# Kernel tuning notes

Measured on AMD Instinct MI355X. Metric: run time of the kernel, lower is better.

Reference implementation:

```python
import jax, jax.numpy as jnp
import numpy as np

B, S, D, H = 4, 2048, 1024, 16
DK = D // H


def setup_inputs() -> dict:
    key = jax.random.key(0)
    ks = jax.random.split(key, 7)
    s = 1.0 / np.sqrt(D)
    return {
        "q": jax.random.normal(ks[0], (B, S, D), jnp.float32),
        "k": jax.random.normal(ks[1], (B, S, D), jnp.float32),
        "v": jax.random.normal(ks[2], (B, S, D), jnp.float32),
        "Wq": jax.random.normal(ks[3], (D, D), jnp.float32) * s,
        "Wk": jax.random.normal(ks[4], (D, D), jnp.float32) * s,
        "Wv": jax.random.normal(ks[5], (D, D), jnp.float32) * s,
        "Wo": jax.random.normal(ks[6], (D, D), jnp.float32) * s,
    }


def _split(x):
    # [B,S,D] -> [B,H,S,DK]
    return x.reshape(B, S, H, DK).transpose(0, 2, 1, 3)


def reference(q, k, v, Wq, Wk, Wv, Wo):
    # Linear projections (nn.Linear with bias=False: x @ W^T)
    qh = _split(q @ Wq.T)
    kh = _split(k @ Wk.T)
    vh = _split(v @ Wv.T)
    scale = 1.0 / jnp.sqrt(jnp.asarray(DK, qh.dtype))
    # attention scores [B,H,S,S]
    attn = jnp.einsum("bhqd,bhkd->bhqk", qh, kh) * scale
    # causal mask: disallow k > q
    causal = jnp.tril(jnp.ones((S, S), dtype=bool))
    attn = jnp.where(causal[None, None], attn, -jnp.inf)
    attn = jax.nn.softmax(attn, axis=-1)  # dropout p=0.0 -> identity
    out = jnp.einsum("bhqk,bhkd->bhqd", attn, vh)
    # combine heads [B,H,S,DK] -> [B,S,D]
    out = out.transpose(0, 2, 1, 3).reshape(B, S, D)
    return out @ Wo.T
```

## Files before the change

kernel.cpp:

```cpp
#include <hip/hip_runtime.h>
#include <math.h>
#include <stdint.h>

#define B_  4
#define S_  2048
#define D_  1024
#define H_  16
#define DK_ 64
#define NR_ (B_ * S_)

typedef _Float16 half8  __attribute__((ext_vector_type(8)));
typedef _Float16 half4  __attribute__((ext_vector_type(4)));
typedef float    floatx4 __attribute__((ext_vector_type(4)));

#define GBN 128
#define GBM 64
#define GBK 32
#define LDH 40

__global__ __launch_bounds__(256)
void gemm_xwt_mfma(const float* __restrict__ X, const float* __restrict__ W,
                   void* __restrict__ outp, int mode) {
    __shared__ __align__(16) _Float16 Xhi[GBN][LDH];
    __shared__ __align__(16) _Float16 Xlo[GBN][LDH];
    __shared__ __align__(16) _Float16 Whi[GBM][LDH];
    __shared__ __align__(16) _Float16 Wlo[GBM][LDH];
    const int K = D_;

    const int tid  = threadIdx.x;
    const int wave = tid >> 6;
    const int lane = tid & 63;
    const int row16 = lane & 15;
    const int quad  = lane >> 4;
    const int n0 = blockIdx.x * GBN;
    const int m0 = blockIdx.y * GBM;

    floatx4 acc[2][4];
    const floatx4 zero4 = {0.f, 0.f, 0.f, 0.f};
    #pragma unroll
    for (int i = 0; i < 2; ++i)
        #pragma unroll
        for (int j = 0; j < 4; ++j) acc[i][j] = zero4;

    for (int k0 = 0; k0 < K; k0 += GBK) {
        __syncthreads();
        #pragma unroll
        for (int i = 0; i < 4; ++i) {
            const int t   = i * 256 + tid;
            const int row = t >> 3;
            const int c4  = (t & 7) << 2;
            float4 xv = *(const float4*)(X + (size_t)(n0 + row) * K + k0 + c4);
            float f[4] = {xv.x, xv.y, xv.z, xv.w};
            #pragma unroll
            for (int c = 0; c < 4; ++c) {
                _Float16 h = (_Float16)f[c];
                Xhi[row][c4 + c] = h;
                Xlo[row][c4 + c] = (_Float16)(f[c] - (float)h);
            }
        }
        #pragma unroll
        for (int i = 0; i < 2; ++i) {
            const int t   = i * 256 + tid;
            const int row = t >> 3;
            const int c4  = (t & 7) << 2;
            float4 wv = *(const float4*)(W + (size_t)(m0 + row) * K + k0 + c4);
            float f[4] = {wv.x, wv.y, wv.z, wv.w};
            #pragma unroll
            for (int c = 0; c < 4; ++c) {
                _Float16 h = (_Float16)f[c];
                Whi[row][c4 + c] = h;
                Wlo[row][c4 + c] = (_Float16)(f[c] - (float)h);
            }
        }
        __syncthreads();

        half8 a_hi[2], a_lo[2], b_hi[4], b_lo[4];
        #pragma unroll
        for (int ni = 0; ni < 2; ++ni) {
            const int r = wave * 32 + ni * 16 + row16;
            a_hi[ni] = *(const half8*)&Xhi[r][quad * 8];
            a_lo[ni] = *(const half8*)&Xlo[r][quad * 8];
        }
        #pragma unroll
        for (int mj = 0; mj < 4; ++mj) {
            const int r = mj * 16 + row16;
            b_hi[mj] = *(const half8*)&Whi[r][quad * 8];
            b_lo[mj] = *(const half8*)&Wlo[r][quad * 8];
        }

        #pragma unroll
        for (int ni = 0; ni < 2; ++ni)
            #pragma unroll
            for (int mj = 0; mj < 4; ++mj) {
                acc[ni][mj] = __builtin_amdgcn_mfma_f32_16x16x32_f16(
                    a_hi[ni], b_hi[mj], acc[ni][mj], 0, 0, 0);
                acc[ni][mj] = __builtin_amdgcn_mfma_f32_16x16x32_f16(
                    a_hi[ni], b_lo[mj], acc[ni][mj], 0, 0, 0);
                acc[ni][mj] = __builtin_amdgcn_mfma_f32_16x16x32_f16(
                    a_lo[ni], b_hi[mj], acc[ni][mj], 0, 0, 0);
            }
    }

    #pragma unroll
    for (int ni = 0; ni < 2; ++ni)
        #pragma unroll
        for (int mj = 0; mj < 4; ++mj) {
            if (mode == 2) {
                const int s  = n0 + wave * 32 + ni * 16 + quad * 4;
                const int b  = s >> 11;
                const int sr = s & (S_ - 1);
                const int m  = m0 + mj * 16 + row16;
                const int h  = m >> 6;
                const int dk = m & 63;
                float4 v4 = make_float4(acc[ni][mj][0], acc[ni][mj][1],
                                        acc[ni][mj][2], acc[ni][mj][3]);
                *(float4*)((float*)outp +
                           (((size_t)b * H_ + h) * DK_ + dk) * S_ + sr) = v4;
            } else {
                #pragma unroll
                for (int rg = 0; rg < 4; ++rg) {
                    const int n = n0 + wave * 32 + ni * 16 + quad * 4 + rg;
                    const int m = m0 + mj * 16 + row16;
                    const float v = acc[ni][mj][rg];
                    if (mode == 0) {
                        ((float*)outp)[(size_t)n * D_ + m] = v;
                    } else {
                        const int b  = n >> 11;
                        const int s  = n & (S_ - 1);
                        const int h  = m >> 6;
                        const int dk = m & 63;
                        union { _Float16 h16; uint16_t u; } hi, lo;
                        hi.h16 = (_Float16)v;
                        lo.h16 = (_Float16)(v - (float)hi.h16);
                        uint32_t u = ((uint32_t)lo.u << 16) | (uint32_t)hi.u;
                        ((uint32_t*)outp)[(((size_t)b * H_ + h) * S_ + s) * DK_ + dk] = u;
                    }
                }
            }
        }
}

__global__ __launch_bounds__(256)
void attn_mfma(const uint32_t* __restrict__ Qhl, const uint32_t* __restrict__ Khl,
               const float* __restrict__ Vt, float* __restrict__ A) {
    __shared__ __align__(16) _Float16 KhiC[64][64];
    __shared__ __align__(16) _Float16 KloC[64][64];
    __shared__ __align__(16) _Float16 VC[64][64];
    __shared__ __align__(16) _Float16 PCT[4][16][72];

    const int bh = blockIdx.y;
    const int qt = (int)(gridDim.x - 1) - (int)blockIdx.x;
    const int q0 = qt * 64;
    const int tid  = threadIdx.x;
    const int wave = tid >> 6;
    const int lane = tid & 63;
    const int c    = lane & 15;
    const int quad = lane >> 4;

    const uint32_t* Kb = Khl + (size_t)bh * S_ * DK_;
    const float*    Vb = Vt  + (size_t)bh * DK_ * S_;

    half8 qhi[2], qlo[2];
    {
        const uint32_t* Qrow = Qhl + ((size_t)bh * S_ + q0 + wave * 16 + c) * DK_;
        #pragma unroll
        for (int ks = 0; ks < 2; ++ks) {
            uint32_t u[8];
            *(uint4*)&u[0] = *(const uint4*)(Qrow + ks * 32 + quad * 8);
            *(uint4*)&u[4] = *(const uint4*)(Qrow + ks * 32 + quad * 8 + 4);
            union { half8 v; uint16_t s[8]; } hi, lo;
            #pragma unroll
            for (int j = 0; j < 8; ++j) {
                hi.s[j] = (uint16_t)(u[j] & 0xffffu);
                lo.s[j] = (uint16_t)(u[j] >> 16);
            }
            qhi[ks] = hi.v; qlo[ks] = lo.v;
        }
    }

    floatx4 acc_o[4];
    const floatx4 zero4 = {0.f, 0.f, 0.f, 0.f};
    #pragma unroll
    for (int dt = 0; dt < 4; ++dt) acc_o[dt] = zero4;
    float mrun = -INFINITY, lrun = 0.f;

    const int srow = tid >> 2;
    const int soff = (tid & 3) * 16;
    const int ch0  = (tid & 3) * 2;

    uint4 ku[4];
    float4 vf[4];
    auto load_tile = [&](int kt) {
        const uint4* ksrc = (const uint4*)(Kb + (size_t)(kt * 64 + srow) * DK_ + soff);
        ku[0] = ksrc[0]; ku[1] = ksrc[1]; ku[2] = ksrc[2]; ku[3] = ksrc[3];
        const float4* vsrc = (const float4*)(Vb + (size_t)srow * S_ + kt * 64 + soff);
        vf[0] = vsrc[0]; vf[1] = vsrc[1]; vf[2] = vsrc[2]; vf[3] = vsrc[3];
    };
    auto write_tile = [&]() {
        #pragma unroll
        for (int hf = 0; hf < 2; ++hf) {
            const int swz = ((ch0 + hf) ^ (srow & 7)) * 8;
            uint32_t uu[8];
            *(uint4*)&uu[0] = ku[2 * hf];
            *(uint4*)&uu[4] = ku[2 * hf + 1];
            union { half8 v; uint16_t s[8]; } hi, lo;
            #pragma unroll
            for (int j = 0; j < 8; ++j) {
                hi.s[j] = (uint16_t)(uu[j] & 0xffffu);
                lo.s[j] = (uint16_t)(uu[j] >> 16);
            }
            *(half8*)&KhiC[srow][swz] = hi.v;
            *(half8*)&KloC[srow][swz] = lo.v;
            union { half8 v; _Float16 h[8]; } vt;
            float4 a = vf[2 * hf], b = vf[2 * hf + 1];
            vt.h[0] = (_Float16)a.x; vt.h[1] = (_Float16)a.y;
            vt.h[2] = (_Float16)a.z; vt.h[3] = (_Float16)a.w;
            vt.h[4] = (_Float16)b.x; vt.h[5] = (_Float16)b.y;
            vt.h[6] = (_Float16)b.z; vt.h[7] = (_Float16)b.w;
            *(half8*)&VC[srow][swz] = vt.v;
        }
    };

    const int qmy = q0 + wave * 16 + c;
    const floatx4 neg4 = {-INFINITY, -INFINITY, -INFINITY, -INFINITY};

    load_tile(0);
    write_tile();

    for (int kt = 0; kt <= qt; ++kt) {
        const int k0 = kt * 64;
        const bool diag = (kt == qt);
        __syncthreads();
        if (kt < qt) load_tile(kt + 1);

        floatx4 sc[4];
        #pragma unroll
        for (int t = 0; t < 4; ++t) {
            if (diag && t > wave) { sc[t] = neg4; continue; }
            floatx4 s4 = zero4;
            const int krow = t * 16 + c;
            #pragma unroll
            for (int ks = 0; ks < 2; ++ks) {
                const int swz = ((ks * 4 + quad) ^ (krow & 7)) * 8;
                half8 kb = *(const half8*)&KhiC[krow][swz];
                half8 kl = *(const half8*)&KloC[krow][swz];
                s4 = __builtin_amdgcn_mfma_f32_16x16x32_f16(kb, qhi[ks], s4, 0, 0, 0);
                s4 = __builtin_amdgcn_mfma_f32_16x16x32_f16(kl, qhi[ks], s4, 0, 0, 0);
                s4 = __builtin_amdgcn_mfma_f32_16x16x32_f16(kb, qlo[ks], s4, 0, 0, 0);
            }
            #pragma unroll
            for (int r = 0; r < 4; ++r) s4[r] *= 0.125f;
            if (diag && t == wave) {
                #pragma unroll
                for (int r = 0; r < 4; ++r) {
                    const int k = k0 + t * 16 + quad * 4 + r;
                    if (k > qmy) s4[r] = -INFINITY;
                }
            }
            sc[t] = s4;
        }

        float mx = -INFINITY;
        #pragma unroll
        for (int t = 0; t < 4; ++t)
            #pragma unroll
            for (int r = 0; r < 4; ++r) mx = fmaxf(mx, sc[t][r]);
        mx = fmaxf(mx, __shfl_xor(mx, 16));
        mx = fmaxf(mx, __shfl_xor(mx, 32));
        const float mnew  = fmaxf(mrun, mx);
        const float alpha = __expf(mrun - mnew);
        float ls = 0.f;
        #pragma unroll
        for (int t = 0; t < 4; ++t) {
            half4 p4;
            #pragma unroll
            for (int r = 0; r < 4; ++r) {
                const float p = __expf(sc[t][r] - mnew);
                ls += p;
                p4[r] = (_Float16)p;
            }
            *(half4*)&PCT[wave][c][t * 16 + quad * 4] = p4;
        }
        lrun = alpha * lrun + ls;
        mrun = mnew;
        #pragma unroll
        for (int dt = 0; dt < 4; ++dt)
            #pragma unroll
            for (int r = 0; r < 4; ++r) acc_o[dt][r] *= alpha;

        #pragma unroll
        for (int kc = 0; kc < 2; ++kc) {
            if (diag && kc == 1 && wave < 2) continue;
            half8 pb = *(const half8*)&PCT[wave][c][kc * 32 + quad * 8];
            #pragma unroll
            for (int dt = 0; dt < 4; ++dt) {
                const int vrow = dt * 16 + c;
                const int swz = ((kc * 4 + quad) ^ (vrow & 7)) * 8;
                half8 va = *(const half8*)&VC[vrow][swz];
                acc_o[dt] = __builtin_amdgcn_mfma_f32_16x16x32_f16(va, pb, acc_o[dt], 0, 0, 0);
            }
        }

        __syncthreads();
        if (kt < qt) write_tile();
    }

    float l = lrun;
    l += __shfl_xor(l, 16);
    l += __shfl_xor(l, 32);
    const float inv = 1.f / l;
    const int b = bh >> 4, h = bh & 15;
    float* dst = A + ((size_t)b * S_ + qmy) * D_ + h * DK_;
    #pragma unroll
    for (int dt = 0; dt < 4; ++dt) {
        float4 o4 = make_float4(acc_o[dt][0] * inv, acc_o[dt][1] * inv,
                                acc_o[dt][2] * inv, acc_o[dt][3] * inv);
        *(float4*)(dst + dt * 16 + quad * 4) = o4;
    }
}

extern "C" void kernel_launch(void* const* d_in, const int* in_sizes, int n_in,
                              void* d_out, int out_size, void* d_ws, size_t ws_size,
                              hipStream_t stream) {
    const float* q  = (const float*)d_in[0];
    const float* k  = (const float*)d_in[1];
    const float* v  = (const float*)d_in[2];
    const float* Wq = (const float*)d_in[3];
    const float* Wk = (const float*)d_in[4];
    const float* Wv = (const float*)d_in[5];
    const float* Wo = (const float*)d_in[6];
    float* out = (float*)d_out;

    const size_t SZ = (size_t)B_ * S_ * D_;
    float* wsf = (float*)d_ws;
    uint32_t* Qhl = (uint32_t*)wsf;
    uint32_t* Khl = (uint32_t*)(wsf + SZ);
    float*    Vt  = wsf + 2 * SZ;
    float*    A   = wsf + 3 * SZ;

    dim3 gb(NR_ / GBN, D_ / GBM);
    gemm_xwt_mfma<<<gb, 256, 0, stream>>>(q, Wq, Qhl, 1);
    gemm_xwt_mfma<<<gb, 256, 0, stream>>>(k, Wk, Khl, 1);
    gemm_xwt_mfma<<<gb, 256, 0, stream>>>(v, Wv, Vt, 2);

    dim3 ga(S_ / 64, B_ * H_);
    attn_mfma<<<ga, 256, 0, stream>>>(Qhl, Khl, Vt, A);

    gemm_xwt_mfma<<<gb, 256, 0, stream>>>(A, Wo, out, 0);
}
```

Baseline: 697.7 us.

## Pre-split inputs to fp16 hi/lo in separate kernels and prefetch GEMM tiles

Adds a split kernel that converts fp32 activations and weights into separate fp16 hi and lo arrays, so the GEMM no longer converts inside its main loop and can load fp16 tiles directly, with register prefetch of the next K tile. Intermediates (Q/K hi-lo, V transposed, attention output hi-lo) are stored as planar fp16, which halves V storage and removes unpacking in the attention kernel. The cost is seven extra split launches and extra global round-trips for the split activations, plus V rounded to fp16 at the GEMM output.

```diff
diff --git a/kernel.cpp b/kernel.cpp
--- a/kernel.cpp
+++ b/kernel.cpp
@@ -13,14 +13,35 @@
 typedef _Float16 half4  __attribute__((ext_vector_type(4)));
 typedef float    floatx4 __attribute__((ext_vector_type(4)));
 
+__global__ __launch_bounds__(256)
+void split_f32(const float* __restrict__ src, _Float16* __restrict__ hi,
+               _Float16* __restrict__ lo, int n8) {
+    const int i = blockIdx.x * 256 + threadIdx.x;
+    if (i >= n8) return;
+    const float4* s4 = (const float4*)src;
+    float4 a = s4[2 * i];
+    float4 b = s4[2 * i + 1];
+    float f[8] = {a.x, a.y, a.z, a.w, b.x, b.y, b.z, b.w};
+    union { half8 v; _Float16 h[8]; } H, L;
+    #pragma unroll
+    for (int j = 0; j < 8; ++j) {
+        _Float16 h = (_Float16)f[j];
+        H.h[j] = h;
+        L.h[j] = (_Float16)(f[j] - (float)h);
+    }
+    *(half8*)(hi + (size_t)i * 8) = H.v;
+    *(half8*)(lo + (size_t)i * 8) = L.v;
+}
+
 #define GBN 128
 #define GBM 64
 #define GBK 32
 #define LDH 40
 
 __global__ __launch_bounds__(256)
-void gemm_xwt_mfma(const float* __restrict__ X, const float* __restrict__ W,
-                   void* __restrict__ outp, int mode) {
+void gemm_xwt_mfma(const _Float16* __restrict__ Xh, const _Float16* __restrict__ Xl,
+                   const _Float16* __restrict__ Wh, const _Float16* __restrict__ Wl,
+                   void* __restrict__ out0, void* __restrict__ out1, int mode) {
     __shared__ __align__(16) _Float16 Xhi[GBN][LDH];
     __shared__ __align__(16) _Float16 Xlo[GBN][LDH];
     __shared__ __align__(16) _Float16 Whi[GBM][LDH];
@@ -35,6 +56,11 @@
     const int n0 = blockIdx.x * GBN;
     const int m0 = blockIdx.y * GBM;
 
+    const int xrow = tid >> 1;
+    const int xc   = (tid & 1) << 4;
+    const int wrow = tid >> 2;
+    const int wc   = (tid & 3) << 3;
+
     floatx4 acc[2][4];
     const floatx4 zero4 = {0.f, 0.f, 0.f, 0.f};
     #pragma unroll
@@ -42,37 +68,31 @@
         #pragma unroll
         for (int j = 0; j < 4; ++j) acc[i][j] = zero4;
 
+    uint4 xh0, xh1, xl0, xl1, wh0, wl0;
+    auto load_regs = [&](int k0) {
+        const _Float16* ph = Xh + (size_t)(n0 + xrow) * K + k0 + xc;
+        const _Float16* pl = Xl + (size_t)(n0 + xrow) * K + k0 + xc;
+        xh0 = *(const uint4*)ph;
+        xh1 = *(const uint4*)(ph + 8);
+        xl0 = *(const uint4*)pl;
+        xl1 = *(const uint4*)(pl + 8);
+        const _Float16* pwh = Wh + (size_t)(m0 + wrow) * K + k0 + wc;
+        const _Float16* pwl = Wl + (size_t)(m0 + wrow) * K + k0 + wc;
+        wh0 = *(const uint4*)pwh;
+        wl0 = *(const uint4*)pwl;
+    };
+
+    load_regs(0);
     for (int k0 = 0; k0 < K; k0 += GBK) {
         __syncthreads();
-        #pragma unroll
-        for (int i = 0; i < 4; ++i) {
-            const int t   = i * 256 + tid;
-            const int row = t >> 3;
-            const int c4  = (t & 7) << 2;
-            float4 xv = *(const float4*)(X + (size_t)(n0 + row) * K + k0 + c4);
-            float f[4] = {xv.x, xv.y, xv.z, xv.w};
-            #pragma unroll
-            for (int c = 0; c < 4; ++c) {
-                _Float16 h = (_Float16)f[c];
-                Xhi[row][c4 + c] = h;
-                Xlo[row][c4 + c] = (_Float16)(f[c] - (float)h);
-            }
-        }
-        #pragma unroll
-        for (int i = 0; i < 2; ++i) {
-            const int t   = i * 256 + tid;
-            const int row = t >> 3;
-            const int c4  = (t & 7) << 2;
-            float4 wv = *(const float4*)(W + (size_t)(m0 + row) * K + k0 + c4);
-            float f[4] = {wv.x, wv.y, wv.z, wv.w};
-            #pragma unroll
-            for (int c = 0; c < 4; ++c) {
-                _Float16 h = (_Float16)f[c];
-                Whi[row][c4 + c] = h;
-                Wlo[row][c4 + c] = (_Float16)(f[c] - (float)h);
-            }
-        }
+        *(uint4*)&Xhi[xrow][xc]     = xh0;
+        *(uint4*)&Xhi[xrow][xc + 8] = xh1;
+        *(uint4*)&Xlo[xrow][xc]     = xl0;
+        *(uint4*)&Xlo[xrow][xc + 8] = xl1;
+        *(uint4*)&Whi[wrow][wc]     = wh0;
+        *(uint4*)&Wlo[wrow][wc]     = wl0;
         __syncthreads();
+        if (k0 + GBK < K) load_regs(k0 + GBK);
 
         half8 a_hi[2], a_lo[2], b_hi[4], b_lo[4];
         #pragma unroll
@@ -112,10 +132,11 @@
                 const int m  = m0 + mj * 16 + row16;
                 const int h  = m >> 6;
                 const int dk = m & 63;
-                float4 v4 = make_float4(acc[ni][mj][0], acc[ni][mj][1],
-                                        acc[ni][mj][2], acc[ni][mj][3]);
-                *(float4*)((float*)outp +
-                           (((size_t)b * H_ + h) * DK_ + dk) * S_ + sr) = v4;
+                half4 h4;
+                #pragma unroll
+                for (int r = 0; r < 4; ++r) h4[r] = (_Float16)acc[ni][mj][r];
+                *(half4*)((_Float16*)out0 +
+                          (((size_t)b * H_ + h) * DK_ + dk) * S_ + sr) = h4;
             } else {
                 #pragma unroll
                 for (int rg = 0; rg < 4; ++rg) {
@@ -123,17 +144,17 @@
                     const int m = m0 + mj * 16 + row16;
                     const float v = acc[ni][mj][rg];
                     if (mode == 0) {
-                        ((float*)outp)[(size_t)n * D_ + m] = v;
+                        ((float*)out0)[(size_t)n * D_ + m] = v;
                     } else {
                         const int b  = n >> 11;
                         const int s  = n & (S_ - 1);
                         const int h  = m >> 6;
                         const int dk = m & 63;
-                        union { _Float16 h16; uint16_t u; } hi, lo;
-                        hi.h16 = (_Float16)v;
-                        lo.h16 = (_Float16)(v - (float)hi.h16);
-                        uint32_t u = ((uint32_t)lo.u << 16) | (uint32_t)hi.u;
-                        ((uint32_t*)outp)[(((size_t)b * H_ + h) * S_ + s) * DK_ + dk] = u;
+                        _Float16 hi16 = (_Float16)v;
+                        _Float16 lo16 = (_Float16)(v - (float)hi16);
+                        const size_t idx = (((size_t)b * H_ + h) * S_ + s) * DK_ + dk;
+                        ((_Float16*)out0)[idx] = hi16;
+                        ((_Float16*)out1)[idx] = lo16;
                     }
                 }
             }
@@ -141,8 +162,10 @@
 }
 
 __global__ __launch_bounds__(256)
-void attn_mfma(const uint32_t* __restrict__ Qhl, const uint32_t* __restrict__ Khl,
-               const float* __restrict__ Vt, float* __restrict__ A) {
+void attn_mfma(const _Float16* __restrict__ Qhi_g, const _Float16* __restrict__ Qlo_g,
+               const _Float16* __restrict__ Khi_g, const _Float16* __restrict__ Klo_g,
+               const _Float16* __restrict__ Vth,
+               _Float16* __restrict__ Ahi, _Float16* __restrict__ Alo) {
     __shared__ __align__(16) _Float16 KhiC[64][64];
     __shared__ __align__(16) _Float16 KloC[64][64];
     __shared__ __align__(16) _Float16 VC[64][64];
@@ -157,24 +180,18 @@
     const int c    = lane & 15;
     const int quad = lane >> 4;
 
-    const uint32_t* Kb = Khl + (size_t)bh * S_ * DK_;
-    const float*    Vb = Vt  + (size_t)bh * DK_ * S_;
+    const _Float16* Kbh = Khi_g + (size_t)bh * S_ * DK_;
+    const _Float16* Kbl = Klo_g + (size_t)bh * S_ * DK_;
+    const _Float16* Vb  = Vth   + (size_t)bh * DK_ * S_;
 
     half8 qhi[2], qlo[2];
     {
-        const uint32_t* Qrow = Qhl + ((size_t)bh * S_ + q0 + wave * 16 + c) * DK_;
+        const _Float16* Qrh = Qhi_g + ((size_t)bh * S_ + q0 + wave * 16 + c) * DK_;
+        const _Float16* Qrl = Qlo_g + ((size_t)bh * S_ + q0 + wave * 16 + c) * DK_;
         #pragma unroll
         for (int ks = 0; ks < 2; ++ks) {
-            uint32_t u[8];
-            *(uint4*)&u[0] = *(const uint4*)(Qrow + ks * 32 + quad * 8);
-            *(uint4*)&u[4] = *(const uint4*)(Qrow + ks * 32 + quad * 8 + 4);
-            union { half8 v; uint16_t s[8]; } hi, lo;
-            #pragma unroll
-            for (int j = 0; j < 8; ++j) {
-                hi.s[j] = (uint16_t)(u[j] & 0xffffu);
-                lo.s[j] = (uint16_t)(u[j] >> 16);
-            }
-            qhi[ks] = hi.v; qlo[ks] = lo.v;
+            qhi[ks] = *(const half8*)(Qrh + ks * 32 + quad * 8);
+            qlo[ks] = *(const half8*)(Qrl + ks * 32 + quad * 8);
         }
     }
 
@@ -188,36 +205,22 @@
     const int soff = (tid & 3) * 16;
     const int ch0  = (tid & 3) * 2;
 
-    uint4 ku[4];
-    float4 vf[4];
+    uint4 kh[2], kl[2], vv[2];
     auto load_tile = [&](int kt) {
-        const uint4* ksrc = (const uint4*)(Kb + (size_t)(kt * 64 + srow) * DK_ + soff);
-        ku[0] = ksrc[0]; ku[1] = ksrc[1]; ku[2] = ksrc[2]; ku[3] = ksrc[3];
-        const float4* vsrc = (const float4*)(Vb + (size_t)srow * S_ + kt * 64 + soff);
-        vf[0] = vsrc[0]; vf[1] = vsrc[1]; vf[2] = vsrc[2]; vf[3] = vsrc[3];
+        const uint4* ph = (const uint4*)(Kbh + (size_t)(kt * 64 + srow) * DK_ + soff);
+        kh[0] = ph[0]; kh[1] = ph[1];
+        const uint4* pl = (const uint4*)(Kbl + (size_t)(kt * 64 + srow) * DK_ + soff);
+        kl[0] = pl[0]; kl[1] = pl[1];
+        const uint4* pv = (const uint4*)(Vb + (size_t)srow * S_ + kt * 64 + soff);
+        vv[0] = pv[0]; vv[1] = pv[1];
     };
     auto write_tile = [&]() {
         #pragma unroll
         for (int hf = 0; hf < 2; ++hf) {
             const int swz = ((ch0 + hf) ^ (srow & 7)) * 8;
-            uint32_t uu[8];
-            *(uint4*)&uu[0] = ku[2 * hf];
-            *(uint4*)&uu[4] = ku[2 * hf + 1];
-            union { half8 v; uint16_t s[8]; } hi, lo;
-            #pragma unroll
-            for (int j = 0; j < 8; ++j) {
-                hi.s[j] = (uint16_t)(uu[j] & 0xffffu);
-                lo.s[j] = (uint16_t)(uu[j] >> 16);
-            }
-            *(half8*)&KhiC[srow][swz] = hi.v;
-            *(half8*)&KloC[srow][swz] = lo.v;
-            union { half8 v; _Float16 h[8]; } vt;
-            float4 a = vf[2 * hf], b = vf[2 * hf + 1];
-            vt.h[0] = (_Float16)a.x; vt.h[1] = (_Float16)a.y;
-            vt.h[2] = (_Float16)a.z; vt.h[3] = (_Float16)a.w;
-            vt.h[4] = (_Float16)b.x; vt.h[5] = (_Float16)b.y;
-            vt.h[6] = (_Float16)b.z; vt.h[7] = (_Float16)b.w;
-            *(half8*)&VC[srow][swz] = vt.v;
+            *(uint4*)&KhiC[srow][swz] = kh[hf];
+            *(uint4*)&KloC[srow][swz] = kl[hf];
+            *(uint4*)&VC[srow][swz]   = vv[hf];
         }
     };
 
@@ -243,9 +246,9 @@
             for (int ks = 0; ks < 2; ++ks) {
                 const int swz = ((ks * 4 + quad) ^ (krow & 7)) * 8;
                 half8 kb = *(const half8*)&KhiC[krow][swz];
-                half8 kl = *(const half8*)&KloC[krow][swz];
+                half8 klo8 = *(const half8*)&KloC[krow][swz];
                 s4 = __builtin_amdgcn_mfma_f32_16x16x32_f16(kb, qhi[ks], s4, 0, 0, 0);
-                s4 = __builtin_amdgcn_mfma_f32_16x16x32_f16(kl, qhi[ks], s4, 0, 0, 0);
+                s4 = __builtin_amdgcn_mfma_f32_16x16x32_f16(klo8, qhi[ks], s4, 0, 0, 0);
                 s4 = __builtin_amdgcn_mfma_f32_16x16x32_f16(kb, qlo[ks], s4, 0, 0, 0);
             }
             #pragma unroll
@@ -310,12 +313,19 @@
     l += __shfl_xor(l, 32);
     const float inv = 1.f / l;
     const int b = bh >> 4, h = bh & 15;
-    float* dst = A + ((size_t)b * S_ + qmy) * D_ + h * DK_;
+    _Float16* dh = Ahi + ((size_t)b * S_ + qmy) * D_ + h * DK_;
+    _Float16* dl = Alo + ((size_t)b * S_ + qmy) * D_ + h * DK_;
     #pragma unroll
     for (int dt = 0; dt < 4; ++dt) {
-        float4 o4 = make_float4(acc_o[dt][0] * inv, acc_o[dt][1] * inv,
-                                acc_o[dt][2] * inv, acc_o[dt][3] * inv);
-        *(float4*)(dst + dt * 16 + quad * 4) = o4;
+        half4 hh, ll;
+        #pragma unroll
+        for (int r = 0; r < 4; ++r) {
+            const float o = acc_o[dt][r] * inv;
+            hh[r] = (_Float16)o;
+            ll[r] = (_Float16)(o - (float)hh[r]);
+        }
+        *(half4*)(dh + dt * 16 + quad * 4) = hh;
+        *(half4*)(dl + dt * 16 + quad * 4) = ll;
     }
 }
 
@@ -331,20 +341,41 @@
     const float* Wo = (const float*)d_in[6];
     float* out = (float*)d_out;
 
-    const size_t SZ = (size_t)B_ * S_ * D_;
-    float* wsf = (float*)d_ws;
-    uint32_t* Qhl = (uint32_t*)wsf;
-    uint32_t* Khl = (uint32_t*)(wsf + SZ);
-    float*    Vt  = wsf + 2 * SZ;
-    float*    A   = wsf + 3 * SZ;
-
+    const size_t SZ  = (size_t)B_ * S_ * D_;
+    const size_t WSZ = (size_t)D_ * D_;
+
+    _Float16* ws  = (_Float16*)d_ws;
+    _Float16* xhi = ws;
+    _Float16* xlo = xhi + SZ;
+    _Float16* whi = xlo + SZ;
+    _Float16* wlo = whi + WSZ;
+    _Float16* Qhi = wlo + WSZ;
+    _Float16* Qlo = Qhi + SZ;
+    _Float16* Khi = Qlo + SZ;
+    _Float16* Klo = Khi + SZ;
+    _Float16* Vth = Klo + SZ;
+    _Float16* Ahi = xhi;
+    _Float16* Alo = xlo;
+
+    const int nx8 = (int)(SZ / 8);
+    const int nw8 = (int)(WSZ / 8);
     dim3 gb(NR_ / GBN, D_ / GBM);
-    gemm_xwt_mfma<<<gb, 256, 0, stream>>>(q, Wq, Qhl, 1);
-    gemm_xwt_mfma<<<gb, 256, 0, stream>>>(k, Wk, Khl, 1);
-    gemm_xwt_mfma<<<gb, 256, 0, stream>>>(v, Wv, Vt, 2);
-
     dim3 ga(S_ / 64, B_ * H_);
-    attn_mfma<<<ga, 256, 0, stream>>>(Qhl, Khl, Vt, A);
-
-    gemm_xwt_mfma<<<gb, 256, 0, stream>>>(A, Wo, out, 0);
+
+    split_f32<<<nw8 / 256, 256, 0, stream>>>(Wq, whi, wlo, nw8);
+    split_f32<<<nx8 / 256, 256, 0, stream>>>(q, xhi, xlo, nx8);
+    gemm_xwt_mfma<<<gb, 256, 0, stream>>>(xhi, xlo, whi, wlo, Qhi, Qlo, 1);
+
+    split_f32<<<nw8 / 256, 256, 0, stream>>>(Wk, whi, wlo, nw8);
+    split_f32<<<nx8 / 256, 256, 0, stream>>>(k, xhi, xlo, nx8);
+    gemm_xwt_mfma<<<gb, 256, 0, stream>>>(xhi, xlo, whi, wlo, Khi, Klo, 1);
+
+    split_f32<<<nw8 / 256, 256, 0, stream>>>(Wv, whi, wlo, nw8);
+    split_f32<<<nx8 / 256, 256, 0, stream>>>(v, xhi, xlo, nx8);
+    gemm_xwt_mfma<<<gb, 256, 0, stream>>>(xhi, xlo, whi, wlo, Vth, nullptr, 2);
+
+    attn_mfma<<<ga, 256, 0, stream>>>(Qhi, Qlo, Khi, Klo, Vth, Ahi, Alo);
+
+    split_f32<<<nw8 / 256, 256, 0, stream>>>(Wo, whi, wlo, nw8);
+    gemm_xwt_mfma<<<gb, 256, 0, stream>>>(Ahi, Alo, whi, wlo, out, nullptr, 0);
 }
```

Result: slower. 896.4 us (+28.5%).
